# Kernel tuning notes

Hardware: AMD Instinct MI355X
Metric: run time of the kernel (lower is better)

The kernel has to match this reference:

```python
import jax, jax.numpy as jnp
import numpy as np

EMBED = 32
HEADS = 8
HEAD_DIM = EMBED // HEADS  # 4


def setup_inputs() -> dict:
    key = jax.random.key(0)
    ks = jax.random.split(key, 12)
    N, Q, K = 4, 2048, 2048
    inp = {
        "query": jax.random.normal(ks[0], (N, Q, EMBED), dtype=jnp.float32),
        "key": jax.random.normal(ks[1], (N, K, EMBED), dtype=jnp.float32),
        "value": jax.random.normal(ks[2], (N, K, EMBED), dtype=jnp.float32),
        "mask": jnp.ones((N, 1, Q, K), dtype=jnp.int32),
        # nn.Linear params: W stored as (in, out) here; math y = x @ W + b
        "Wq": jax.random.normal(ks[3], (EMBED, EMBED), dtype=jnp.float32) / np.sqrt(EMBED),
        "bq": jax.random.normal(ks[4], (EMBED,), dtype=jnp.float32) * 0.01,
        "Wk": jax.random.normal(ks[5], (EMBED, EMBED), dtype=jnp.float32) / np.sqrt(EMBED),
        "bk": jax.random.normal(ks[6], (EMBED,), dtype=jnp.float32) * 0.01,
        "Wv": jax.random.normal(ks[7], (EMBED, EMBED), dtype=jnp.float32) / np.sqrt(EMBED),
        "bv": jax.random.normal(ks[8], (EMBED,), dtype=jnp.float32) * 0.01,
        "Wo": jax.random.normal(ks[9], (EMBED, EMBED), dtype=jnp.float32) / np.sqrt(EMBED),
        "bo": jax.random.normal(ks[10], (EMBED,), dtype=jnp.float32) * 0.01,
    }
    return inp


def reference(query, key, value, mask, Wq, bq, Wk, bk, Wv, bv, Wo, bo):
    N, Qlen, _ = query.shape
    Klen = key.shape[1]
    # linear projections
    q = (query @ Wq + bq).reshape(N, Qlen, HEADS, HEAD_DIM)
    k = (key @ Wk + bk).reshape(N, Klen, HEADS, HEAD_DIM)
    v = (value @ Wv + bv).reshape(N, Klen, HEADS, HEAD_DIM)
    # energy: [N, H, Q, K]
    energy = jnp.einsum("nqhd,nkhd->nhqk", q, k)
    energy = jnp.where(mask == 0, jnp.float32(-1e20), energy)
    # NOTE: original scales by sqrt(embedSize), not sqrt(headDim)
    attn = jax.nn.softmax(energy / jnp.sqrt(jnp.float32(EMBED)), axis=3)
    out = jnp.einsum("nhqv,nvhd->nqhd", attn, v).reshape(N, Qlen, EMBED)
    return out @ Wo + bo
```

## Files before the change

kernel.cpp:

```cpp
#include <hip/hip_runtime.h>

#define NB 4
#define SEQ 2048
#define EMB 32
#define HEADS 8
#define HD 4

typedef float v2f __attribute__((ext_vector_type(2)));
typedef unsigned int uint;

__device__ __forceinline__ v2f splat2(float x) { v2f r; r.x = x; r.y = x; return r; }
__device__ __forceinline__ v2f pkfma(v2f a, v2f b, v2f c) {
  return __builtin_elementwise_fma(a, b, c);
}

__global__ __launch_bounds__(256) void mask_pack_kernel(
    const int* __restrict__ mask, uint* __restrict__ pmw) {
  int g = blockIdx.x * 256 + threadIdx.x;
  const int4 v = ((const int4*)mask)[g];
  uint nib = (uint)(v.x != 0) | ((uint)(v.y != 0) << 1) |
             ((uint)(v.z != 0) << 2) | ((uint)(v.w != 0) << 3);
  int lane = threadIdx.x & 63;
  uint w = nib << (4 * (lane & 7));
  w |= __shfl_xor(w, 1);
  w |= __shfl_xor(w, 2);
  w |= __shfl_xor(w, 4);
  if ((lane & 7) == 0) pmw[g >> 3] = w;
}

__global__ __launch_bounds__(256) void proj_kv_kernel(
    const float* __restrict__ key, const float* __restrict__ value,
    const float* __restrict__ Wk, const float* __restrict__ bk,
    const float* __restrict__ Wv, const float* __restrict__ bv,
    float* __restrict__ Kp, float* __restrict__ Vp) {
  const int half = NB * SEQ / 8;
  bool isV = blockIdx.x >= half;
  const float* X = isV ? value : key;
  const float* W = isV ? Wv : Wk;
  const float* b = isV ? bv : bk;
  float* P = isV ? Vp : Kp;
  int blk = isV ? (blockIdx.x - half) : blockIdx.x;

  __shared__ float sW[EMB][EMB];
  __shared__ float sb[EMB];
  __shared__ float sX[8][EMB];
  int t = threadIdx.x;
  for (int i = t; i < EMB * EMB; i += 256) sW[i >> 5][i & 31] = W[i];
  if (t < EMB) sb[t] = b[t];
  size_t row0 = (size_t)blk * 8;
  int r = t >> 5, c = t & 31;
  sX[r][c] = X[(row0 + r) * EMB + c];
  __syncthreads();
  float acc = sb[c];
#pragma unroll
  for (int d = 0; d < EMB; ++d) acc = fmaf(sX[r][d], sW[d][c], acc);
  P[(row0 + r) * EMB + c] = acc;
}

__device__ __forceinline__ void load_tile(
    const float*& kptr, const float*& vptr, const uint*& mwp,
    float4 (&KK)[4], float4 (&VV)[4], uint4& MW) {
  KK[0] = *(const float4*)(kptr);
  KK[1] = *(const float4*)(kptr + EMB);
  KK[2] = *(const float4*)(kptr + 2 * EMB);
  KK[3] = *(const float4*)(kptr + 3 * EMB);
  VV[0] = *(const float4*)(vptr);
  VV[1] = *(const float4*)(vptr + EMB);
  VV[2] = *(const float4*)(vptr + 2 * EMB);
  VV[3] = *(const float4*)(vptr + 3 * EMB);
  MW.x = mwp[0];
  MW.y = mwp[64];
  MW.z = mwp[128];
  MW.w = mwp[192];
  kptr += 32 * EMB; vptr += 32 * EMB; mwp += 1;
}

__device__ __forceinline__ void compute_tile(
    const float4 (&KK)[4], const float4 (&VV)[4], const uint4& MW, int ks4,
    const v2f (&q2)[2][4], v2f (&l2)[2], v2f (&ac2)[2][4]) {
  v2f pf[2][4];
#pragma unroll
  for (int p = 0; p < 2; ++p) {
#pragma unroll
    for (int j = 0; j < 4; ++j) {
      const float4 kk = KK[j];
      v2f s = pkfma(q2[p][0], splat2(kk.x),
              pkfma(q2[p][1], splat2(kk.y),
              pkfma(q2[p][2], splat2(kk.z), q2[p][3] * splat2(kk.w))));
      pf[p][j].x = __builtin_amdgcn_exp2f(s.x);
      pf[p][j].y = __builtin_amdgcn_exp2f(s.y);
    }
  }
  uint allm = MW.x & MW.y & MW.z & MW.w;
  if (allm != 0xFFFFFFFFu) {
#pragma unroll
    for (int j = 0; j < 4; ++j) {
      if (!((MW.x >> (ks4 + j)) & 1u)) pf[0][j].x = 0.0f;
      if (!((MW.y >> (ks4 + j)) & 1u)) pf[0][j].y = 0.0f;
      if (!((MW.z >> (ks4 + j)) & 1u)) pf[1][j].x = 0.0f;
      if (!((MW.w >> (ks4 + j)) & 1u)) pf[1][j].y = 0.0f;
    }
  }
#pragma unroll
  for (int p = 0; p < 2; ++p) {
    l2[p] += (pf[p][0] + pf[p][1]) + (pf[p][2] + pf[p][3]);
#pragma unroll
    for (int j = 0; j < 4; ++j) {
      const float4 vv = VV[j];
      ac2[p][0] = pkfma(pf[p][j], splat2(vv.x), ac2[p][0]);
      ac2[p][1] = pkfma(pf[p][j], splat2(vv.y), ac2[p][1]);
      ac2[p][2] = pkfma(pf[p][j], splat2(vv.z), ac2[p][2]);
      ac2[p][3] = pkfma(pf[p][j], splat2(vv.w), ac2[p][3]);
    }
  }
}

__global__ __launch_bounds__(256, 2) void attn_kernel(
    const float* __restrict__ query, const uint* __restrict__ pmw,
    const float* __restrict__ Kp, const float* __restrict__ Vp,
    const float* __restrict__ Wq, const float* __restrict__ bq,
    const float* __restrict__ Wo, const float* __restrict__ bo,
    float* __restrict__ out) {
  __shared__ float sWq[EMB][EMB];
  __shared__ float sWo[EMB][EMB];
  __shared__ float sbq[EMB];
  __shared__ float sbo[EMB];
  __shared__ float sX[16][EMB];
  __shared__ float sCtx[16][EMB + 1];

  int t = threadIdx.x;
  int n = blockIdx.x >> 7;
  int qt = blockIdx.x & 127;
  int qrow0 = qt * 16;

  int rl = t >> 6;
  int lane = t & 63;
  int h = lane & 7;
  int ks = lane >> 3;
  int ks4 = 4 * ks;

  for (int i = t; i < EMB * EMB; i += 256) {
    sWq[i >> 5][i & 31] = Wq[i];
    sWo[i >> 5][i & 31] = Wo[i];
  }
  if (t < EMB) { sbq[t] = bq[t]; sbo[t] = bo[t]; }
  {
    int r = t >> 5, c = t & 31;
    sX[r][c] = query[((size_t)n * SEQ + qrow0 + r) * EMB + c];
    sX[r + 8][c] = query[((size_t)n * SEQ + qrow0 + r + 8) * EMB + c];
  }
  __syncthreads();

  const float SC = 0.17677669529663687f * 1.4426950408889634f;
  float q[4][4];
#pragma unroll
  for (int r = 0; r < 4; ++r)
#pragma unroll
    for (int d = 0; d < 4; ++d) q[r][d] = sbq[4 * h + d];
#pragma unroll
  for (int j = 0; j < EMB; ++j) {
    float w0 = sWq[j][4 * h + 0], w1 = sWq[j][4 * h + 1];
    float w2 = sWq[j][4 * h + 2], w3 = sWq[j][4 * h + 3];
#pragma unroll
    for (int r = 0; r < 4; ++r) {
      float x = sX[4 * rl + r][j];
      q[r][0] = fmaf(x, w0, q[r][0]);
      q[r][1] = fmaf(x, w1, q[r][1]);
      q[r][2] = fmaf(x, w2, q[r][2]);
      q[r][3] = fmaf(x, w3, q[r][3]);
    }
  }
  v2f q2[2][4];
#pragma unroll
  for (int p = 0; p < 2; ++p)
#pragma unroll
    for (int d = 0; d < 4; ++d) {
      q2[p][d].x = q[2 * p][d] * SC;
      q2[p][d].y = q[2 * p + 1][d] * SC;
    }

  const float* kptr = Kp + (size_t)n * SEQ * EMB + (size_t)ks4 * EMB + 4 * h;
  const float* vptr = Vp + (size_t)n * SEQ * EMB + (size_t)ks4 * EMB + 4 * h;
  size_t rb = (size_t)n * SEQ + qrow0 + 4 * rl;
  const uint* mwp = pmw + rb * (SEQ / 32);

  v2f l2[2], ac2[2][4];
#pragma unroll
  for (int p = 0; p < 2; ++p) {
    l2[p] = splat2(0.0f);
#pragma unroll
    for (int d = 0; d < 4; ++d) ac2[p][d] = splat2(0.0f);
  }

  float4 ka[4], va[4]; uint4 ma;
  float4 kb[4], vb[4]; uint4 mb;
  load_tile(kptr, vptr, mwp, ka, va, ma);
  for (int i = 0; i < 31; ++i) {
    load_tile(kptr, vptr, mwp, kb, vb, mb);
    compute_tile(ka, va, ma, ks4, q2, l2, ac2);
    load_tile(kptr, vptr, mwp, ka, va, ma);
    compute_tile(kb, vb, mb, ks4, q2, l2, ac2);
  }
  load_tile(kptr, vptr, mwp, kb, vb, mb);
  compute_tile(ka, va, ma, ks4, q2, l2, ac2);
  compute_tile(kb, vb, mb, ks4, q2, l2, ac2);

#pragma unroll
  for (int d = 8; d <= 32; d <<= 1) {
#pragma unroll
    for (int p = 0; p < 2; ++p) {
      l2[p].x += __shfl_xor(l2[p].x, d);
      l2[p].y += __shfl_xor(l2[p].y, d);
#pragma unroll
      for (int e = 0; e < 4; ++e) {
        ac2[p][e].x += __shfl_xor(ac2[p][e].x, d);
        ac2[p][e].y += __shfl_xor(ac2[p][e].y, d);
      }
    }
  }

  if (ks < 4) {
#pragma unroll
    for (int p = 0; p < 2; ++p) {
      float invA = __builtin_amdgcn_rcpf(l2[p].x);
      float invB = __builtin_amdgcn_rcpf(l2[p].y);
      float vA = (ks == 0) ? ac2[p][0].x : (ks == 1) ? ac2[p][1].x
               : (ks == 2) ? ac2[p][2].x : ac2[p][3].x;
      float vB = (ks == 0) ? ac2[p][0].y : (ks == 1) ? ac2[p][1].y
               : (ks == 2) ? ac2[p][2].y : ac2[p][3].y;
      sCtx[4 * rl + 2 * p + 0][4 * h + ks] = vA * invA;
      sCtx[4 * rl + 2 * p + 1][4 * h + ks] = vB * invB;
    }
  }
  __syncthreads();

  int e = t & 31;
#pragma unroll
  for (int rr = 0; rr < 2; ++rr) {
    int r = (t >> 5) + 8 * rr;
    float o = sbo[e];
#pragma unroll
    for (int j = 0; j < EMB; ++j) o = fmaf(sCtx[r][j], sWo[j][e], o);
    out[((size_t)n * SEQ + qrow0 + r) * EMB + e] = o;
  }
}

extern "C" void kernel_launch(void* const* d_in, const int* in_sizes, int n_in,
                              void* d_out, int out_size, void* d_ws, size_t ws_size,
                              hipStream_t stream) {
  const float* query = (const float*)d_in[0];
  const float* key   = (const float*)d_in[1];
  const float* value = (const float*)d_in[2];
  const int*   mask  = (const int*)d_in[3];
  const float* Wq = (const float*)d_in[4];
  const float* bq = (const float*)d_in[5];
  const float* Wk = (const float*)d_in[6];
  const float* bk = (const float*)d_in[7];
  const float* Wv = (const float*)d_in[8];
  const float* bv = (const float*)d_in[9];
  const float* Wo = (const float*)d_in[10];
  const float* bo = (const float*)d_in[11];
  float* out = (float*)d_out;

  float* Kp = (float*)d_ws;
  float* Vp = Kp + (size_t)NB * SEQ * EMB;
  uint* pmw = (uint*)(Vp + (size_t)NB * SEQ * EMB);

  mask_pack_kernel<<<dim3(NB * SEQ * SEQ / 4 / 256), dim3(256), 0, stream>>>(
      mask, pmw);
  proj_kv_kernel<<<dim3(2 * NB * SEQ / 8), dim3(256), 0, stream>>>(
      key, value, Wk, bk, Wv, bv, Kp, Vp);
  attn_kernel<<<dim3(NB * (SEQ / 16)), dim3(256), 0, stream>>>(
      query, pmw, Kp, Vp, Wq, bq, Wo, bo, out);
}
```

Before: 67.87 us.

## Split attention key range across two waves per row group and merge mask/proj kernels

New measurement: 255.9 us. 277% more time.

```diff
diff --git a/kernel.cpp b/kernel.cpp
--- a/kernel.cpp
+++ b/kernel.cpp
@@ -14,47 +14,49 @@
   return __builtin_elementwise_fma(a, b, c);
 }
 
-__global__ __launch_bounds__(256) void mask_pack_kernel(
-    const int* __restrict__ mask, uint* __restrict__ pmw) {
-  int g = blockIdx.x * 256 + threadIdx.x;
-  const int4 v = ((const int4*)mask)[g];
-  uint nib = (uint)(v.x != 0) | ((uint)(v.y != 0) << 1) |
-             ((uint)(v.z != 0) << 2) | ((uint)(v.w != 0) << 3);
-  int lane = threadIdx.x & 63;
-  uint w = nib << (4 * (lane & 7));
-  w |= __shfl_xor(w, 1);
-  w |= __shfl_xor(w, 2);
-  w |= __shfl_xor(w, 4);
-  if ((lane & 7) == 0) pmw[g >> 3] = w;
-}
-
-__global__ __launch_bounds__(256) void proj_kv_kernel(
+__global__ __launch_bounds__(256) void pack_proj_kernel(
+    const int* __restrict__ mask, uint* __restrict__ pmw,
     const float* __restrict__ key, const float* __restrict__ value,
     const float* __restrict__ Wk, const float* __restrict__ bk,
     const float* __restrict__ Wv, const float* __restrict__ bv,
     float* __restrict__ Kp, float* __restrict__ Vp) {
-  const int half = NB * SEQ / 8;
-  bool isV = blockIdx.x >= half;
-  const float* X = isV ? value : key;
-  const float* W = isV ? Wv : Wk;
-  const float* b = isV ? bv : bk;
-  float* P = isV ? Vp : Kp;
-  int blk = isV ? (blockIdx.x - half) : blockIdx.x;
-
-  __shared__ float sW[EMB][EMB];
-  __shared__ float sb[EMB];
-  __shared__ float sX[8][EMB];
-  int t = threadIdx.x;
-  for (int i = t; i < EMB * EMB; i += 256) sW[i >> 5][i & 31] = W[i];
-  if (t < EMB) sb[t] = b[t];
-  size_t row0 = (size_t)blk * 8;
-  int r = t >> 5, c = t & 31;
-  sX[r][c] = X[(row0 + r) * EMB + c];
-  __syncthreads();
-  float acc = sb[c];
-#pragma unroll
-  for (int d = 0; d < EMB; ++d) acc = fmaf(sX[r][d], sW[d][c], acc);
-  P[(row0 + r) * EMB + c] = acc;
+  const int packBlocks = NB * SEQ * SEQ / 4 / 256;
+  if (blockIdx.x < packBlocks) {
+    int g = blockIdx.x * 256 + threadIdx.x;
+    const int4 v = ((const int4*)mask)[g];
+    uint nib = (uint)(v.x != 0) | ((uint)(v.y != 0) << 1) |
+               ((uint)(v.z != 0) << 2) | ((uint)(v.w != 0) << 3);
+    int lane = threadIdx.x & 63;
+    uint w = nib << (4 * (lane & 7));
+    w |= __shfl_xor(w, 1);
+    w |= __shfl_xor(w, 2);
+    w |= __shfl_xor(w, 4);
+    if ((lane & 7) == 0) pmw[g >> 3] = w;
+  } else {
+    const int half = NB * SEQ / 8;
+    int blk2 = blockIdx.x - packBlocks;
+    bool isV = blk2 >= half;
+    const float* X = isV ? value : key;
+    const float* W = isV ? Wv : Wk;
+    const float* b = isV ? bv : bk;
+    float* P = isV ? Vp : Kp;
+    int blk = isV ? (blk2 - half) : blk2;
+
+    __shared__ float sW[EMB][EMB];
+    __shared__ float sb[EMB];
+    __shared__ float sX[8][EMB];
+    int t = threadIdx.x;
+    for (int i = t; i < EMB * EMB; i += 256) sW[i >> 5][i & 31] = W[i];
+    if (t < EMB) sb[t] = b[t];
+    size_t row0 = (size_t)blk * 8;
+    int r = t >> 5, c = t & 31;
+    sX[r][c] = X[(row0 + r) * EMB + c];
+    __syncthreads();
+    float acc = sb[c];
+#pragma unroll
+    for (int d = 0; d < EMB; ++d) acc = fmaf(sX[r][d], sW[d][c], acc);
+    P[(row0 + r) * EMB + c] = acc;
+  }
 }
 
 __device__ __forceinline__ void load_tile(
@@ -115,7 +117,7 @@
   }
 }
 
-__global__ __launch_bounds__(256, 2) void attn_kernel(
+__global__ __launch_bounds__(512, 4) void attn_kernel(
     const float* __restrict__ query, const uint* __restrict__ pmw,
     const float* __restrict__ Kp, const float* __restrict__ Vp,
     const float* __restrict__ Wq, const float* __restrict__ bq,
@@ -127,19 +129,23 @@
   __shared__ float sbo[EMB];
   __shared__ float sX[16][EMB];
   __shared__ float sCtx[16][EMB + 1];
+  __shared__ float sPart[2][16][EMB];
+  __shared__ float sL[2][16][HEADS];
 
   int t = threadIdx.x;
   int n = blockIdx.x >> 7;
   int qt = blockIdx.x & 127;
   int qrow0 = qt * 16;
 
-  int rl = t >> 6;
+  int w = t >> 6;
+  int quad = w >> 1;
+  int khalf = w & 1;
   int lane = t & 63;
   int h = lane & 7;
   int ks = lane >> 3;
   int ks4 = 4 * ks;
 
-  for (int i = t; i < EMB * EMB; i += 256) {
+  for (int i = t; i < EMB * EMB; i += 512) {
     sWq[i >> 5][i & 31] = Wq[i];
     sWo[i >> 5][i & 31] = Wo[i];
   }
@@ -147,7 +153,6 @@
   {
     int r = t >> 5, c = t & 31;
     sX[r][c] = query[((size_t)n * SEQ + qrow0 + r) * EMB + c];
-    sX[r + 8][c] = query[((size_t)n * SEQ + qrow0 + r + 8) * EMB + c];
   }
   __syncthreads();
 
@@ -163,7 +168,7 @@
     float w2 = sWq[j][4 * h + 2], w3 = sWq[j][4 * h + 3];
 #pragma unroll
     for (int r = 0; r < 4; ++r) {
-      float x = sX[4 * rl + r][j];
+      float x = sX[4 * quad + r][j];
       q[r][0] = fmaf(x, w0, q[r][0]);
       q[r][1] = fmaf(x, w1, q[r][1]);
       q[r][2] = fmaf(x, w2, q[r][2]);
@@ -179,10 +184,12 @@
       q2[p][d].y = q[2 * p + 1][d] * SC;
     }
 
-  const float* kptr = Kp + (size_t)n * SEQ * EMB + (size_t)ks4 * EMB + 4 * h;
-  const float* vptr = Vp + (size_t)n * SEQ * EMB + (size_t)ks4 * EMB + 4 * h;
-  size_t rb = (size_t)n * SEQ + qrow0 + 4 * rl;
-  const uint* mwp = pmw + rb * (SEQ / 32);
+  const float* kptr = Kp + (size_t)n * SEQ * EMB + (size_t)khalf * 1024 * EMB
+                         + (size_t)ks4 * EMB + 4 * h;
+  const float* vptr = Vp + (size_t)n * SEQ * EMB + (size_t)khalf * 1024 * EMB
+                         + (size_t)ks4 * EMB + 4 * h;
+  size_t rb = (size_t)n * SEQ + qrow0 + 4 * quad;
+  const uint* mwp = pmw + rb * (SEQ / 32) + khalf * 32;
 
   v2f l2[2], ac2[2][4];
 #pragma unroll
@@ -195,7 +202,7 @@
   float4 ka[4], va[4]; uint4 ma;
   float4 kb[4], vb[4]; uint4 mb;
   load_tile(kptr, vptr, mwp, ka, va, ma);
-  for (int i = 0; i < 31; ++i) {
+  for (int i = 0; i < 15; ++i) {
     load_tile(kptr, vptr, mwp, kb, vb, mb);
     compute_tile(ka, va, ma, ks4, q2, l2, ac2);
     load_tile(kptr, vptr, mwp, ka, va, ma);
@@ -219,25 +226,33 @@
     }
   }
 
-  if (ks < 4) {
-#pragma unroll
-    for (int p = 0; p < 2; ++p) {
-      float invA = __builtin_amdgcn_rcpf(l2[p].x);
-      float invB = __builtin_amdgcn_rcpf(l2[p].y);
+#pragma unroll
+  for (int p = 0; p < 2; ++p) {
+    int r0 = 4 * quad + 2 * p;
+    if (ks < 4) {
       float vA = (ks == 0) ? ac2[p][0].x : (ks == 1) ? ac2[p][1].x
                : (ks == 2) ? ac2[p][2].x : ac2[p][3].x;
       float vB = (ks == 0) ? ac2[p][0].y : (ks == 1) ? ac2[p][1].y
                : (ks == 2) ? ac2[p][2].y : ac2[p][3].y;
-      sCtx[4 * rl + 2 * p + 0][4 * h + ks] = vA * invA;
-      sCtx[4 * rl + 2 * p + 1][4 * h + ks] = vB * invB;
+      sPart[khalf][r0 + 0][4 * h + ks] = vA;
+      sPart[khalf][r0 + 1][4 * h + ks] = vB;
+    } else if (ks == 4) {
+      sL[khalf][r0 + 0][h] = l2[p].x;
+      sL[khalf][r0 + 1][h] = l2[p].y;
     }
   }
   __syncthreads();
 
-  int e = t & 31;
-#pragma unroll
-  for (int rr = 0; rr < 2; ++rr) {
-    int r = (t >> 5) + 8 * rr;
+  {
+    int r = t >> 5, c = t & 31, hh = c >> 2;
+    float num = sPart[0][r][c] + sPart[1][r][c];
+    float den = sL[0][r][hh] + sL[1][r][hh];
+    sCtx[r][c] = num * __builtin_amdgcn_rcpf(den);
+  }
+  __syncthreads();
+
+  {
+    int r = t >> 5, e = t & 31;
     float o = sbo[e];
 #pragma unroll
     for (int j = 0; j < EMB; ++j) o = fmaf(sCtx[r][j], sWo[j][e], o);
@@ -266,10 +281,10 @@
   float* Vp = Kp + (size_t)NB * SEQ * EMB;
   uint* pmw = (uint*)(Vp + (size_t)NB * SEQ * EMB);
 
-  mask_pack_kernel<<<dim3(NB * SEQ * SEQ / 4 / 256), dim3(256), 0, stream>>>(
-      mask, pmw);
-  proj_kv_kernel<<<dim3(2 * NB * SEQ / 8), dim3(256), 0, stream>>>(
-      key, value, Wk, bk, Wv, bv, Kp, Vp);
-  attn_kernel<<<dim3(NB * (SEQ / 16)), dim3(256), 0, stream>>>(
+  const int packBlocks = NB * SEQ * SEQ / 4 / 256;
+  const int projBlocks = 2 * NB * SEQ / 8;
+  pack_proj_kernel<<<dim3(packBlocks + projBlocks), dim3(256), 0, stream>>>(
+      mask, pmw, key, value, Wk, bk, Wv, bv, Kp, Vp);
+  attn_kernel<<<dim3(NB * (SEQ / 16)), dim3(512), 0, stream>>>(
       query, pmw, Kp, Vp, Wq, bq, Wo, bo, out);
 }
```
